# Optimization experiments

Hardware: AMD Instinct MI355X
Metric: run time of the kernel (lower is better)

Reference implementation:

```python
import jax, jax.numpy as jnp
import numpy as np

BS, C_IN, S1 = 64, 256, 32
D_OUT, J = 32, 10          # out_dim, num_out_caps (as_final_output -> spatial_size_2)
I = S1 * S1                # num_in_caps = 1024
ROUTE_NUM = 3


def setup_inputs() -> dict:
    key = jax.random.key(0)
    k1, k2, k3 = jax.random.split(key, 3)
    x = jax.random.normal(k1, (BS, C_IN, S1, S1), dtype=jnp.float32)
    W = jax.random.normal(k2, (D_OUT * J, C_IN), dtype=jnp.float32) * 0.02  # 1x1 conv weight
    W_b = jax.random.normal(k3, (D_OUT * J,), dtype=jnp.float32) * 0.02     # conv bias
    return {"x": x, "W": W, "W_b": W_b}


def squash(vec):
    # vec: [bs, j, d]; coeff = ||v||^2 / (1+||v||^2) / ||v||
    norm = jnp.linalg.norm(vec, axis=2, keepdims=True)
    norm_sq = norm * norm
    return vec * (norm_sq / (1.0 + norm_sq) / norm)


def reference(x, W, W_b):
    bs = x.shape[0]
    # 1x1 conv == per-pixel matmul: [bs, J*D, h, w]
    pred = jnp.einsum('bchw,oc->bohw', x, W) + W_b[None, :, None, None]
    # torch: resize(bs, J, D, I) on contiguous tensor, then permute(0,3,1,2)
    pred = pred.reshape(bs, J, D_OUT, I).transpose(0, 3, 1, 2)  # [bs, I, J, D]
    b = jnp.zeros((bs, J, I), dtype=x.dtype)  # b_init='zero'
    v = None
    for _ in range(ROUTE_NUM):
        c = jax.nn.softmax(b, axis=1)                    # softmax over output caps j
        s = jnp.einsum('bji,bijd->bjd', c, pred)          # per-capsule weighted sum
        v = squash(s)                                     # [bs, J, D]
        delta_b = jnp.einsum('bjd,bijd->bji', v, pred)    # agreement
        b = b + jax.lax.stop_gradient(delta_b)            # torch .detach()
    return v  # as_final_output=True -> [bs, J, D]
```

## Files before the change

kernel.cpp:

```cpp
#include <hip/hip_runtime.h>
#include <hip/hip_bf16.h>

typedef __attribute__((ext_vector_type(8))) unsigned short u16x8;
typedef __attribute__((ext_vector_type(4))) unsigned short u16x4;
typedef __attribute__((ext_vector_type(8))) short short8;
typedef __attribute__((ext_vector_type(4))) float floatx4;

#define BS 64
#define CIN 256
#define II 1024
#define OO 320
#define JJ 10
#define DD 32

__device__ __forceinline__ float b2f(unsigned short u) {
    union { unsigned int i; float f; } x; x.i = ((unsigned int)u) << 16; return x.f;
}
__device__ __forceinline__ unsigned short f2b(float f) {
    union { float f; unsigned int i; } x; x.f = f;
    unsigned int r = x.i + 0x7fffu + ((x.i >> 16) & 1u);
    return (unsigned short)(r >> 16);
}

__device__ __forceinline__ float butterfly32(const float* p, int l) {
    float q16[16];
#pragma unroll
    for (int d = 0; d < 16; ++d) {
        float keep = (l & 1) ? p[2 * d + 1] : p[2 * d];
        float send = (l & 1) ? p[2 * d] : p[2 * d + 1];
        q16[d] = keep + __shfl_xor(send, 1);
    }
    float q8[8];
#pragma unroll
    for (int d = 0; d < 8; ++d) {
        float keep = (l & 2) ? q16[2 * d + 1] : q16[2 * d];
        float send = (l & 2) ? q16[2 * d] : q16[2 * d + 1];
        q8[d] = keep + __shfl_xor(send, 2);
    }
    float q4[4];
#pragma unroll
    for (int d = 0; d < 4; ++d) {
        float keep = (l & 4) ? q8[2 * d + 1] : q8[2 * d];
        float send = (l & 4) ? q8[2 * d] : q8[2 * d + 1];
        q4[d] = keep + __shfl_xor(send, 4);
    }
    float q2[2];
#pragma unroll
    for (int d = 0; d < 2; ++d) {
        float keep = (l & 8) ? q4[2 * d + 1] : q4[2 * d];
        float send = (l & 8) ? q4[2 * d] : q4[2 * d + 1];
        q2[d] = keep + __shfl_xor(send, 8);
    }
    float keep = (l & 16) ? q2[1] : q2[0];
    float send = (l & 16) ? q2[0] : q2[1];
    float q1 = keep + __shfl_xor(send, 16);
    q1 += __shfl_xor(q1, 32);
    return q1;
}

__global__ __launch_bounds__(256) void k_prepW(const float* __restrict__ W,
                                               unsigned short* __restrict__ Wl) {
    int gid = blockIdx.x * 256 + threadIdx.x;
    int lm = gid & 15;
    int quad = (gid >> 4) & 3;
    int mtl = (gid >> 6) & 3;
    int ks = (gid >> 8) & 7;
    int oc = gid >> 11;
    const float* src = W + (size_t)(oc * 64 + mtl * 16 + lm) * CIN + ks * 32 + quad * 8;
    float4 v0 = *(const float4*)src;
    float4 v1 = *(const float4*)(src + 4);
    u16x8 u;
    u[0] = f2b(v0.x); u[1] = f2b(v0.y); u[2] = f2b(v0.z); u[3] = f2b(v0.w);
    u[4] = f2b(v1.x); u[5] = f2b(v1.y); u[6] = f2b(v1.z); u[7] = f2b(v1.w);
    *(u16x8*)(Wl + (size_t)gid * 8) = u;
}

__global__ __launch_bounds__(512) void k_gemm8(const float* __restrict__ x,
                                               const unsigned short* __restrict__ Wl,
                                               const float* __restrict__ Wb,
                                               unsigned short* __restrict__ pred,
                                               float* __restrict__ psumC) {
    __shared__ unsigned short buf[2][16896];
    __shared__ float Wb_lds[OO];

    const int ic = blockIdx.x, b = blockIdx.y;
    const int t = threadIdx.x, w = t >> 6, l = t & 63;
    const int lm = l & 15, quad = l >> 4;
    const int i0 = ic * 128;

    if (t < OO) Wb_lds[t] = Wb[t];

    {
        const u16x8* src = (const u16x8*)Wl;
        u16x8* dst = (u16x8*)buf[1];
        dst[t] = src[t];
        dst[t + 512] = src[t + 512];
        dst[t + 1024] = src[t + 1024];
        dst[t + 1536] = src[t + 1536];
    }

    short8 bfrag[8];
    float csum[2];
    const int crow = t >> 5, f4 = t & 31;
    const int cs_c = t >> 2, cs_seg = t & 3;
#pragma unroll
    for (int kc = 0; kc < 2; ++kc) {
        float4 fr[8];
#pragma unroll
        for (int p = 0; p < 8; ++p) {
            int c = kc * 128 + p * 16 + crow;
            fr[p] = *(const float4*)(x + ((size_t)b * CIN + c) * II + i0 + 4 * f4);
        }
#pragma unroll
        for (int p = 0; p < 8; ++p) {
            int cl = p * 16 + crow;
            u16x4 u;
            u[0] = f2b(fr[p].x); u[1] = f2b(fr[p].y); u[2] = f2b(fr[p].z); u[3] = f2b(fr[p].w);
            *(u16x4*)&buf[0][cl * 132 + 4 * f4] = u;
        }
        __syncthreads();
#pragma unroll
        for (int k2 = 0; k2 < 4; ++k2) {
            short8 f;
#pragma unroll
            for (int j = 0; j < 8; ++j)
                f[j] = (short)buf[0][(k2 * 32 + quad * 8 + j) * 132 + w * 16 + lm];
            bfrag[kc * 4 + k2] = f;
        }
        {
            float cs = 0.f;
#pragma unroll
            for (int q = 0; q < 8; ++q) {
                u16x4 u = *(const u16x4*)&buf[0][cs_c * 132 + cs_seg * 32 + q * 4];
                cs += b2f(u[0]) + b2f(u[1]) + b2f(u[2]) + b2f(u[3]);
            }
            cs += __shfl_xor(cs, 1);
            cs += __shfl_xor(cs, 2);
            csum[kc] = cs;
        }
        __syncthreads();
    }
    if (cs_seg == 0) {
        size_t cbase = ((size_t)ic * BS + b) * CIN;
        psumC[cbase + cs_c] = csum[0];
        psumC[cbase + 128 + cs_c] = csum[1];
    }

    const size_t predrow = ((size_t)b * II + i0 + w * 16 + lm) * OO;
#pragma unroll 1
    for (int oc = 0; oc < 5; ++oc) {
        if (oc < 4) {
            const u16x8* src = (const u16x8*)Wl + (size_t)(oc + 1) * 2048;
            u16x8* dst = (u16x8*)buf[oc & 1];
            dst[t] = src[t];
            dst[t + 512] = src[t + 512];
            dst[t + 1024] = src[t + 1024];
            dst[t + 1536] = src[t + 1536];
        }
        const unsigned short* ab = buf[(oc + 1) & 1];
        floatx4 acc[4] = {};
#pragma unroll
        for (int ks = 0; ks < 8; ++ks)
#pragma unroll
            for (int mtl = 0; mtl < 4; ++mtl) {
                short8 af = *(const short8*)(ab + (size_t)(((ks * 4 + mtl) * 4 + quad) * 16 + lm) * 8);
                acc[mtl] = __builtin_amdgcn_mfma_f32_16x16x32_bf16(af, bfrag[ks], acc[mtl], 0, 0, 0);
            }
#pragma unroll
        for (int mtl = 0; mtl < 4; ++mtl) {
            int ob = oc * 64 + mtl * 16 + quad * 4;
            u16x4 sv;
#pragma unroll
            for (int r = 0; r < 4; ++r) sv[r] = f2b(acc[mtl][r] + Wb_lds[ob + r]);
            *(u16x4*)(pred + predrow + ob) = sv;
        }
        __syncthreads();
    }
}

__global__ __launch_bounds__(320) void k_gemv(const float* __restrict__ psumC,
                                              const float* __restrict__ W,
                                              const float* __restrict__ Wb,
                                              float* __restrict__ s1) {
    __shared__ float y_lds[CIN];
    const int b = blockIdx.x, t = threadIdx.x;
    if (t < CIN) {
        float s = 0.f;
#pragma unroll
        for (int sl = 0; sl < 8; ++sl) s += psumC[((size_t)sl * BS + b) * CIN + t];
        y_lds[t] = s;
    }
    __syncthreads();
    const float* wr = W + (size_t)t * CIN;
    float acc = 0.f;
#pragma unroll 4
    for (int c = 0; c < CIN; c += 4) {
        float4 wv = *(const float4*)(wr + c);
        acc += wv.x * y_lds[c] + wv.y * y_lds[c + 1] + wv.z * y_lds[c + 2] + wv.w * y_lds[c + 3];
    }
    s1[(size_t)b * OO + t] = 0.1f * (acc + 1024.0f * Wb[t]);
}

__global__ __launch_bounds__(640) void k_route1(const float* __restrict__ s1,
                                                const unsigned short* __restrict__ pred,
                                                float* __restrict__ blogG,
                                                float* __restrict__ psum1) {
    __shared__ float s_lds[OO];
    __shared__ float v_lds[OO];
    __shared__ float cf[JJ];
    __shared__ float dbuf[JJ][128];

    const int ic = blockIdx.x, b = blockIdx.y;
    const int t = threadIdx.x, w = t >> 6, l = t & 63;

    u16x8 va[4], vb[4];
    {
        const unsigned short* p0 = pred + ((size_t)b * II + ic * 128 + 2 * l) * OO + w * DD;
#pragma unroll
        for (int q = 0; q < 4; ++q) {
            va[q] = *(const u16x8*)(p0 + q * 8);
            vb[q] = *(const u16x8*)(p0 + OO + q * 8);
        }
    }

    if (t < OO) s_lds[t] = s1[(size_t)b * OO + t];
    __syncthreads();
    if (t < JJ) {
        float n2 = 0.f;
#pragma unroll
        for (int d = 0; d < DD; ++d) { float v = s_lds[t * DD + d]; n2 += v * v; }
        cf[t] = sqrtf(n2) / (1.0f + n2);
    }
    __syncthreads();
    if (t < OO) v_lds[t] = s_lds[t] * cf[t >> 5];
    __syncthreads();

    float d0 = 0.f, d1 = 0.f;
#pragma unroll
    for (int q = 0; q < 4; ++q)
#pragma unroll
        for (int e = 0; e < 8; ++e) {
            float vv = v_lds[w * DD + q * 8 + e];
            d0 += vv * b2f(va[q][e]);
            d1 += vv * b2f(vb[q][e]);
        }
    *(float2*)(blogG + ((size_t)b * JJ + w) * II + ic * 128 + 2 * l) = make_float2(d0, d1);
    dbuf[w][2 * l] = d0; dbuf[w][2 * l + 1] = d1;
    __syncthreads();

    if (t < 128) {
        float lg[JJ];
#pragma unroll
        for (int j = 0; j < JJ; ++j) lg[j] = dbuf[j][t];
        float m = lg[0];
#pragma unroll
        for (int j = 1; j < JJ; ++j) m = fmaxf(m, lg[j]);
        float Z = 0.f, c[JJ];
#pragma unroll
        for (int j = 0; j < JJ; ++j) { c[j] = __expf(lg[j] - m); Z += c[j]; }
        float inv = 1.0f / Z;
#pragma unroll
        for (int j = 0; j < JJ; ++j) dbuf[j][t] = c[j] * inv;
    }
    __syncthreads();

    float c0 = dbuf[w][2 * l], c1 = dbuf[w][2 * l + 1];
    float p[DD];
#pragma unroll
    for (int q = 0; q < 4; ++q)
#pragma unroll
        for (int e = 0; e < 8; ++e)
            p[q * 8 + e] = c0 * b2f(va[q][e]) + c1 * b2f(vb[q][e]);
    float s = butterfly32(p, l);
    if (l < 32) psum1[((size_t)ic * BS + b) * OO + w * DD + l] = s;
}

__global__ __launch_bounds__(640) void k_route2(const float* __restrict__ psum1,
                                                const unsigned short* __restrict__ pred,
                                                const float* __restrict__ blogG,
                                                float* __restrict__ psum2) {
    __shared__ float s_lds[OO];
    __shared__ float v_lds[OO];
    __shared__ float cf[JJ];
    __shared__ float dbuf[JJ][128];

    const int ic = blockIdx.x, b = blockIdx.y;
    const int t = threadIdx.x, w = t >> 6, l = t & 63;

    u16x8 va[4], vb[4];
    {
        const unsigned short* p0 = pred + ((size_t)b * II + ic * 128 + 2 * l) * OO + w * DD;
#pragma unroll
        for (int q = 0; q < 4; ++q) {
            va[q] = *(const u16x8*)(p0 + q * 8);
            vb[q] = *(const u16x8*)(p0 + OO + q * 8);
        }
    }

    if (t < OO) {
        float s = 0.f;
#pragma unroll
        for (int sl = 0; sl < 8; ++sl) s += psum1[((size_t)sl * BS + b) * OO + t];
        s_lds[t] = s;
    }
    __syncthreads();
    if (t < JJ) {
        float n2 = 0.f;
#pragma unroll
        for (int d = 0; d < DD; ++d) { float v = s_lds[t * DD + d]; n2 += v * v; }
        cf[t] = sqrtf(n2) / (1.0f + n2);
    }
    __syncthreads();
    if (t < OO) v_lds[t] = s_lds[t] * cf[t >> 5];
    __syncthreads();

    float d0 = 0.f, d1 = 0.f;
#pragma unroll
    for (int q = 0; q < 4; ++q)
#pragma unroll
        for (int e = 0; e < 8; ++e) {
            float vv = v_lds[w * DD + q * 8 + e];
            d0 += vv * b2f(va[q][e]);
            d1 += vv * b2f(vb[q][e]);
        }
    float2 bl = *(const float2*)(blogG + ((size_t)b * JJ + w) * II + ic * 128 + 2 * l);
    dbuf[w][2 * l] = bl.x + d0; dbuf[w][2 * l + 1] = bl.y + d1;
    __syncthreads();

    if (t < 128) {
        float lg[JJ];
#pragma unroll
        for (int j = 0; j < JJ; ++j) lg[j] = dbuf[j][t];
        float m = lg[0];
#pragma unroll
        for (int j = 1; j < JJ; ++j) m = fmaxf(m, lg[j]);
        float Z = 0.f, c[JJ];
#pragma unroll
        for (int j = 0; j < JJ; ++j) { c[j] = __expf(lg[j] - m); Z += c[j]; }
        float inv = 1.0f / Z;
#pragma unroll
        for (int j = 0; j < JJ; ++j) dbuf[j][t] = c[j] * inv;
    }
    __syncthreads();

    float c0 = dbuf[w][2 * l], c1 = dbuf[w][2 * l + 1];
    float p[DD];
#pragma unroll
    for (int q = 0; q < 4; ++q)
#pragma unroll
        for (int e = 0; e < 8; ++e)
            p[q * 8 + e] = c0 * b2f(va[q][e]) + c1 * b2f(vb[q][e]);
    float s = butterfly32(p, l);
    if (l < 32) psum2[((size_t)ic * BS + b) * OO + w * DD + l] = s;
}

__global__ __launch_bounds__(320) void k_final2(const float* __restrict__ psum2,
                                                float* __restrict__ out) {
    __shared__ float s_lds[OO];
    __shared__ float cf[JJ];
    int b = blockIdx.x, t = threadIdx.x;
    float s = 0.f;
#pragma unroll
    for (int sl = 0; sl < 8; ++sl) s += psum2[((size_t)sl * BS + b) * OO + t];
    s_lds[t] = s;
    __syncthreads();
    if (t < JJ) {
        float n2 = 0.f;
#pragma unroll
        for (int d = 0; d < DD; ++d) { float v = s_lds[t * DD + d]; n2 += v * v; }
        cf[t] = sqrtf(n2) / (1.0f + n2);
    }
    __syncthreads();
    out[b * OO + t] = s_lds[t] * cf[t >> 5];
}

extern "C" void kernel_launch(void* const* d_in, const int* in_sizes, int n_in,
                              void* d_out, int out_size, void* d_ws, size_t ws_size,
                              hipStream_t stream) {
    const float* x  = (const float*)d_in[0];
    const float* W  = (const float*)d_in[1];
    const float* Wb = (const float*)d_in[2];

    char* ws = (char*)d_ws;
    unsigned short* pred = (unsigned short*)ws;
    unsigned short* Wl   = (unsigned short*)(ws + 41943040);
    float* psumC = (float*)(ws + 42106880);
    float* s1    = (float*)(ws + 42631168);
    float* psum1 = (float*)(ws + 42713088);
    float* psum2 = (float*)(ws + 43368448);
    float* blogG = (float*)(ws + 44023808);

    k_prepW<<<40, 256, 0, stream>>>(W, Wl);
    k_gemm8<<<dim3(8, BS), 512, 0, stream>>>(x, Wl, Wb, pred, psumC);
    k_gemv<<<BS, 320, 0, stream>>>(psumC, W, Wb, s1);
    k_route1<<<dim3(8, BS), 640, 0, stream>>>(s1, pred, blogG, psum1);
    k_route2<<<dim3(8, BS), 640, 0, stream>>>(psum1, pred, blogG, psum2);
    k_final2<<<BS, 320, 0, stream>>>(psum2, (float*)d_out);
}
```

Baseline: 152.2 us.

## Fuse GEMM and routing iterations into one cooperative persistent kernel

Adds a cooperative megakernel that computes the 1x1-conv GEMM, keeps each block's bf16 predictions packed in registers, and runs both routing passes plus the final squash with grid-wide syncs between stages. This avoids writing and re-reading the large pred tensor in global memory, and it replaces several kernel launches with one. The first-iteration sum now comes from per-block partials of pred rather than a separate GEMV. The costs are three grid syncs, higher register pressure from holding 40 packed values per thread, and a reliance on all 512 blocks being co-resident. If the cooperative launch fails, the old kernel sequence runs instead.

```diff
diff --git a/kernel.cpp b/kernel.cpp
--- a/kernel.cpp
+++ b/kernel.cpp
@@ -1,5 +1,8 @@
 #include <hip/hip_runtime.h>
 #include <hip/hip_bf16.h>
+#include <hip/hip_cooperative_groups.h>
+
+namespace cg = cooperative_groups;
 
 typedef __attribute__((ext_vector_type(8))) unsigned short u16x8;
 typedef __attribute__((ext_vector_type(4))) unsigned short u16x4;
@@ -56,6 +59,33 @@
     float q1 = keep + __shfl_xor(send, 16);
     q1 += __shfl_xor(q1, 32);
     return q1;
+}
+
+__device__ __forceinline__ float butterfly16(const float* p, int l) {
+    float q8[8];
+#pragma unroll
+    for (int d = 0; d < 8; ++d) {
+        float keep = (l & 1) ? p[2 * d + 1] : p[2 * d];
+        float send = (l & 1) ? p[2 * d] : p[2 * d + 1];
+        q8[d] = keep + __shfl_xor(send, 1);
+    }
+    float q4[4];
+#pragma unroll
+    for (int d = 0; d < 4; ++d) {
+        float keep = (l & 2) ? q8[2 * d + 1] : q8[2 * d];
+        float send = (l & 2) ? q8[2 * d] : q8[2 * d + 1];
+        q4[d] = keep + __shfl_xor(send, 2);
+    }
+    float q2[2];
+#pragma unroll
+    for (int d = 0; d < 2; ++d) {
+        float keep = (l & 4) ? q4[2 * d + 1] : q4[2 * d];
+        float send = (l & 4) ? q4[2 * d] : q4[2 * d + 1];
+        q2[d] = keep + __shfl_xor(send, 4);
+    }
+    float keep = (l & 8) ? q2[1] : q2[0];
+    float send = (l & 8) ? q2[0] : q2[1];
+    return keep + __shfl_xor(send, 8);
 }
 
 __global__ __launch_bounds__(256) void k_prepW(const float* __restrict__ W,
@@ -75,6 +105,202 @@
     *(u16x8*)(Wl + (size_t)gid * 8) = u;
 }
 
+
+__device__ __forceinline__ void route_pass(
+        const float* __restrict__ srcpart, float scale, bool first,
+        const unsigned* pk, float* b_reg, float* __restrict__ dstpart,
+        float* sacc, float* v_lds, float* cf,
+        int ic, int b, int t, int l, int lm, int quad) {
+    if (t < OO) {
+        float s = 0.f;
+#pragma unroll
+        for (int sl = 0; sl < 8; ++sl) s += srcpart[((size_t)sl * BS + b) * OO + t];
+        sacc[t] = scale * s;
+    }
+    __syncthreads();
+    if (t < JJ) {
+        float n2 = 0.f;
+#pragma unroll
+        for (int d = 0; d < DD; ++d) { float v = sacc[t * DD + d]; n2 += v * v; }
+        cf[t] = sqrtf(n2) / (1.0f + n2);
+    }
+    __syncthreads();
+    if (t < OO) { v_lds[t] = sacc[t] * cf[t >> 5]; sacc[t] = 0.f; }
+    __syncthreads();
+
+    float dj[JJ];
+#pragma unroll
+    for (int j = 0; j < JJ; ++j) dj[j] = 0.f;
+#pragma unroll
+    for (int m = 0; m < 20; ++m) {
+        float4 vv = *(const float4*)&v_lds[m * 16 + quad * 4];
+        unsigned a0 = pk[2 * m], a1 = pk[2 * m + 1];
+        dj[m >> 1] += b2f((unsigned short)(a0 & 0xffffu)) * vv.x
+                    + b2f((unsigned short)(a0 >> 16)) * vv.y
+                    + b2f((unsigned short)(a1 & 0xffffu)) * vv.z
+                    + b2f((unsigned short)(a1 >> 16)) * vv.w;
+    }
+#pragma unroll
+    for (int j = 0; j < JJ; ++j) {
+        float d = dj[j];
+        d += __shfl_xor(d, 16);
+        d += __shfl_xor(d, 32);
+        b_reg[j] = first ? d : (b_reg[j] + d);
+    }
+    float mx = b_reg[0];
+#pragma unroll
+    for (int j = 1; j < JJ; ++j) mx = fmaxf(mx, b_reg[j]);
+    float cj[JJ], Z = 0.f;
+#pragma unroll
+    for (int j = 0; j < JJ; ++j) { cj[j] = __expf(b_reg[j] - mx); Z += cj[j]; }
+    float inv = 1.0f / Z;
+#pragma unroll
+    for (int g = 0; g < 5; ++g) {
+        float v16[16];
+#pragma unroll
+        for (int mm = 0; mm < 4; ++mm) {
+            int m = 4 * g + mm;
+            unsigned a0 = pk[2 * m], a1 = pk[2 * m + 1];
+            float c = cj[m >> 1] * inv;
+            v16[4 * mm + 0] = c * b2f((unsigned short)(a0 & 0xffffu));
+            v16[4 * mm + 1] = c * b2f((unsigned short)(a0 >> 16));
+            v16[4 * mm + 2] = c * b2f((unsigned short)(a1 & 0xffffu));
+            v16[4 * mm + 3] = c * b2f((unsigned short)(a1 >> 16));
+        }
+        float q = butterfly16(v16, l);
+        atomicAdd(&sacc[g * 64 + (lm >> 2) * 16 + quad * 4 + (lm & 3)], q);
+    }
+    __syncthreads();
+    if (t < OO) dstpart[((size_t)ic * BS + b) * OO + t] = sacc[t];
+}
+
+__global__ __launch_bounds__(512, 4) void k_mega(
+        const float* __restrict__ x, const unsigned short* __restrict__ Wl,
+        const float* __restrict__ Wb, float* __restrict__ s1part,
+        float* __restrict__ psum1, float* __restrict__ psum2,
+        float* __restrict__ out) {
+    __shared__ unsigned short buf[2][16896];
+    __shared__ float Wb_lds[OO];
+    __shared__ float sacc[OO];
+    __shared__ __align__(16) float v_lds[OO];
+    __shared__ float cf[16];
+
+    cg::grid_group gg = cg::this_grid();
+
+    const int ic = blockIdx.x, b = blockIdx.y;
+    const int t = threadIdx.x, w = t >> 6, l = t & 63;
+    const int lm = l & 15, quad = l >> 4;
+    const int i0 = ic * 128;
+
+    if (t < OO) { Wb_lds[t] = Wb[t]; sacc[t] = 0.f; }
+
+    {
+        const u16x8* src = (const u16x8*)Wl;
+        u16x8* dst = (u16x8*)buf[1];
+        dst[t] = src[t];
+        dst[t + 512] = src[t + 512];
+        dst[t + 1024] = src[t + 1024];
+        dst[t + 1536] = src[t + 1536];
+    }
+
+    short8 bfrag[8];
+    const int crow = t >> 5, f4 = t & 31;
+#pragma unroll
+    for (int kc = 0; kc < 2; ++kc) {
+        float4 fr[8];
+#pragma unroll
+        for (int p = 0; p < 8; ++p) {
+            int c = kc * 128 + p * 16 + crow;
+            fr[p] = *(const float4*)(x + ((size_t)b * CIN + c) * II + i0 + 4 * f4);
+        }
+#pragma unroll
+        for (int p = 0; p < 8; ++p) {
+            int cl = p * 16 + crow;
+            u16x4 u;
+            u[0] = f2b(fr[p].x); u[1] = f2b(fr[p].y); u[2] = f2b(fr[p].z); u[3] = f2b(fr[p].w);
+            *(u16x4*)&buf[0][cl * 132 + 4 * f4] = u;
+        }
+        __syncthreads();
+#pragma unroll
+        for (int k2 = 0; k2 < 4; ++k2) {
+            short8 f;
+#pragma unroll
+            for (int j = 0; j < 8; ++j)
+                f[j] = (short)buf[0][(k2 * 32 + quad * 8 + j) * 132 + w * 16 + lm];
+            bfrag[kc * 4 + k2] = f;
+        }
+        __syncthreads();
+    }
+
+    unsigned pk[40];
+#pragma unroll
+    for (int oc = 0; oc < 5; ++oc) {
+        if (oc < 4) {
+            const u16x8* src = (const u16x8*)Wl + (size_t)(oc + 1) * 2048;
+            u16x8* dst = (u16x8*)buf[oc & 1];
+            dst[t] = src[t];
+            dst[t + 512] = src[t + 512];
+            dst[t + 1024] = src[t + 1024];
+            dst[t + 1536] = src[t + 1536];
+        }
+        const unsigned short* ab = buf[(oc + 1) & 1];
+        floatx4 acc[4] = {};
+#pragma unroll
+        for (int ks = 0; ks < 8; ++ks)
+#pragma unroll
+            for (int mtl = 0; mtl < 4; ++mtl) {
+                short8 af = *(const short8*)(ab + (size_t)(((ks * 4 + mtl) * 4 + quad) * 16 + lm) * 8);
+                acc[mtl] = __builtin_amdgcn_mfma_f32_16x16x32_bf16(af, bfrag[ks], acc[mtl], 0, 0, 0);
+            }
+        float av[16];
+#pragma unroll
+        for (int mtl = 0; mtl < 4; ++mtl) {
+            int ob = oc * 64 + mtl * 16 + quad * 4;
+#pragma unroll
+            for (int r = 0; r < 4; ++r) av[mtl * 4 + r] = acc[mtl][r] + Wb_lds[ob + r];
+            pk[oc * 8 + mtl * 2 + 0] =
+                (unsigned)f2b(av[mtl * 4 + 0]) | ((unsigned)f2b(av[mtl * 4 + 1]) << 16);
+            pk[oc * 8 + mtl * 2 + 1] =
+                (unsigned)f2b(av[mtl * 4 + 2]) | ((unsigned)f2b(av[mtl * 4 + 3]) << 16);
+        }
+        float q = butterfly16(av, l);
+        atomicAdd(&sacc[oc * 64 + (lm >> 2) * 16 + quad * 4 + (lm & 3)], q);
+        __syncthreads();
+    }
+
+    if (t < OO) s1part[((size_t)ic * BS + b) * OO + t] = sacc[t];
+    __threadfence();
+    gg.sync();
+
+    float b_reg[JJ];
+    route_pass(s1part, 0.1f, true, pk, b_reg, psum1, sacc, v_lds, cf, ic, b, t, l, lm, quad);
+    __threadfence();
+    gg.sync();
+
+    route_pass(psum1, 1.0f, false, pk, b_reg, psum2, sacc, v_lds, cf, ic, b, t, l, lm, quad);
+    __threadfence();
+    gg.sync();
+
+    if (ic == 0) {
+        if (t < OO) {
+            float s = 0.f;
+#pragma unroll
+            for (int sl = 0; sl < 8; ++sl) s += psum2[((size_t)sl * BS + b) * OO + t];
+            sacc[t] = s;
+        }
+        __syncthreads();
+        if (t < JJ) {
+            float n2 = 0.f;
+#pragma unroll
+            for (int d = 0; d < DD; ++d) { float v = sacc[t * DD + d]; n2 += v * v; }
+            cf[t] = sqrtf(n2) / (1.0f + n2);
+        }
+        __syncthreads();
+        if (t < OO) out[b * OO + t] = sacc[t] * cf[t >> 5];
+    }
+}
+
+
 __global__ __launch_bounds__(512) void k_gemm8(const float* __restrict__ x,
                                                const unsigned short* __restrict__ Wl,
                                                const float* __restrict__ Wb,
@@ -389,8 +615,24 @@
     float* psum1 = (float*)(ws + 42713088);
     float* psum2 = (float*)(ws + 43368448);
     float* blogG = (float*)(ws + 44023808);
+    float* s1part = (float*)(ws + 46645248);
 
     k_prepW<<<40, 256, 0, stream>>>(W, Wl);
+
+    {
+        const float* a0 = x;
+        const unsigned short* a1 = Wl;
+        const float* a2 = Wb;
+        float* a3 = s1part;
+        float* a4 = psum1;
+        float* a5 = psum2;
+        float* a6 = (float*)d_out;
+        void* kargs[] = {&a0, &a1, &a2, &a3, &a4, &a5, &a6};
+        hipError_t e = hipLaunchCooperativeKernel(k_mega, dim3(8, BS), dim3(512, 1, 1),
+                                                  kargs, 0, stream);
+        if (e == hipSuccess) return;
+    }
+
     k_gemm8<<<dim3(8, BS), 512, 0, stream>>>(x, Wl, Wb, pred, psumC);
     k_gemv<<<BS, 320, 0, stream>>>(psumC, W, Wb, s1);
     k_route1<<<dim3(8, BS), 640, 0, stream>>>(s1, pred, blogG, psum1);
```

Result: slower. 471.7 us (+209.9%).

## Reorder bf16 pred layout so GEMM stores and routing loads are coalesced

Applied to the files above, without the earlier changes.

The GEMM epilogue now writes pred in a blocked layout: per (batch, 128-capsule chunk), groups of 4 output channels by 128 capsules, each capsule's 4 channels contiguous. The two routing kernels read this layout with 8 strided 16-byte loads whose lanes are adjacent in memory, replacing the row-major [i][320] reads that strode 640 bytes between lanes. The aim is fully coalesced global traffic for the pred tensor, which is written once and read twice. The index math has to stay consistent between producer and consumers.

```diff
diff --git a/kernel.cpp b/kernel.cpp
--- a/kernel.cpp
+++ b/kernel.cpp
@@ -75,6 +75,7 @@
     *(u16x8*)(Wl + (size_t)gid * 8) = u;
 }
 
+
 __global__ __launch_bounds__(512) void k_gemm8(const float* __restrict__ x,
                                                const unsigned short* __restrict__ Wl,
                                                const float* __restrict__ Wb,
@@ -146,7 +147,7 @@
         psumC[cbase + 128 + cs_c] = csum[1];
     }
 
-    const size_t predrow = ((size_t)b * II + i0 + w * 16 + lm) * OO;
+    const size_t predbase = ((size_t)(b * 8 + ic)) * 40960 + (size_t)(w * 16 + lm) * 4;
 #pragma unroll 1
     for (int oc = 0; oc < 5; ++oc) {
         if (oc < 4) {
@@ -169,10 +170,11 @@
 #pragma unroll
         for (int mtl = 0; mtl < 4; ++mtl) {
             int ob = oc * 64 + mtl * 16 + quad * 4;
+            int mprime = oc * 16 + mtl * 4 + quad;
             u16x4 sv;
 #pragma unroll
             for (int r = 0; r < 4; ++r) sv[r] = f2b(acc[mtl][r] + Wb_lds[ob + r]);
-            *(u16x4*)(pred + predrow + ob) = sv;
+            *(u16x4*)(pred + predbase + (size_t)mprime * 512) = sv;
         }
         __syncthreads();
     }
@@ -213,14 +215,13 @@
     const int ic = blockIdx.x, b = blockIdx.y;
     const int t = threadIdx.x, w = t >> 6, l = t & 63;
 
-    u16x8 va[4], vb[4];
+    u16x8 Ld[8];
     {
-        const unsigned short* p0 = pred + ((size_t)b * II + ic * 128 + 2 * l) * OO + w * DD;
-#pragma unroll
-        for (int q = 0; q < 4; ++q) {
-            va[q] = *(const u16x8*)(p0 + q * 8);
-            vb[q] = *(const u16x8*)(p0 + OO + q * 8);
-        }
+        const unsigned short* p0 = pred + ((size_t)(b * 8 + ic)) * 40960
+                                 + (size_t)(w * 8) * 512 + 8 * l;
+#pragma unroll
+        for (int dq = 0; dq < 8; ++dq)
+            Ld[dq] = *(const u16x8*)(p0 + (size_t)dq * 512);
     }
 
     if (t < OO) s_lds[t] = s1[(size_t)b * OO + t];
@@ -237,12 +238,12 @@
 
     float d0 = 0.f, d1 = 0.f;
 #pragma unroll
-    for (int q = 0; q < 4; ++q)
-#pragma unroll
-        for (int e = 0; e < 8; ++e) {
-            float vv = v_lds[w * DD + q * 8 + e];
-            d0 += vv * b2f(va[q][e]);
-            d1 += vv * b2f(vb[q][e]);
+    for (int dq = 0; dq < 8; ++dq)
+#pragma unroll
+        for (int e = 0; e < 4; ++e) {
+            float vv = v_lds[w * DD + dq * 4 + e];
+            d0 += vv * b2f(Ld[dq][e]);
+            d1 += vv * b2f(Ld[dq][4 + e]);
         }
     *(float2*)(blogG + ((size_t)b * JJ + w) * II + ic * 128 + 2 * l) = make_float2(d0, d1);
     dbuf[w][2 * l] = d0; dbuf[w][2 * l + 1] = d1;
@@ -267,10 +268,10 @@
     float c0 = dbuf[w][2 * l], c1 = dbuf[w][2 * l + 1];
     float p[DD];
 #pragma unroll
-    for (int q = 0; q < 4; ++q)
-#pragma unroll
-        for (int e = 0; e < 8; ++e)
-            p[q * 8 + e] = c0 * b2f(va[q][e]) + c1 * b2f(vb[q][e]);
+    for (int dq = 0; dq < 8; ++dq)
+#pragma unroll
+        for (int e = 0; e < 4; ++e)
+            p[dq * 4 + e] = c0 * b2f(Ld[dq][e]) + c1 * b2f(Ld[dq][4 + e]);
     float s = butterfly32(p, l);
     if (l < 32) psum1[((size_t)ic * BS + b) * OO + w * DD + l] = s;
 }
@@ -287,14 +288,13 @@
     const int ic = blockIdx.x, b = blockIdx.y;
     const int t = threadIdx.x, w = t >> 6, l = t & 63;
 
-    u16x8 va[4], vb[4];
+    u16x8 Ld[8];
     {
-        const unsigned short* p0 = pred + ((size_t)b * II + ic * 128 + 2 * l) * OO + w * DD;
-#pragma unroll
-        for (int q = 0; q < 4; ++q) {
-            va[q] = *(const u16x8*)(p0 + q * 8);
-            vb[q] = *(const u16x8*)(p0 + OO + q * 8);
-        }
+        const unsigned short* p0 = pred + ((size_t)(b * 8 + ic)) * 40960
+                                 + (size_t)(w * 8) * 512 + 8 * l;
+#pragma unroll
+        for (int dq = 0; dq < 8; ++dq)
+            Ld[dq] = *(const u16x8*)(p0 + (size_t)dq * 512);
     }
 
     if (t < OO) {
@@ -316,12 +316,12 @@
 
     float d0 = 0.f, d1 = 0.f;
 #pragma unroll
-    for (int q = 0; q < 4; ++q)
-#pragma unroll
-        for (int e = 0; e < 8; ++e) {
-            float vv = v_lds[w * DD + q * 8 + e];
-            d0 += vv * b2f(va[q][e]);
-            d1 += vv * b2f(vb[q][e]);
+    for (int dq = 0; dq < 8; ++dq)
+#pragma unroll
+        for (int e = 0; e < 4; ++e) {
+            float vv = v_lds[w * DD + dq * 4 + e];
+            d0 += vv * b2f(Ld[dq][e]);
+            d1 += vv * b2f(Ld[dq][4 + e]);
         }
     float2 bl = *(const float2*)(blogG + ((size_t)b * JJ + w) * II + ic * 128 + 2 * l);
     dbuf[w][2 * l] = bl.x + d0; dbuf[w][2 * l + 1] = bl.y + d1;
@@ -346,10 +346,10 @@
     float c0 = dbuf[w][2 * l], c1 = dbuf[w][2 * l + 1];
     float p[DD];
 #pragma unroll
-    for (int q = 0; q < 4; ++q)
-#pragma unroll
-        for (int e = 0; e < 8; ++e)
-            p[q * 8 + e] = c0 * b2f(va[q][e]) + c1 * b2f(vb[q][e]);
+    for (int dq = 0; dq < 8; ++dq)
+#pragma unroll
+        for (int e = 0; e < 4; ++e)
+            p[dq * 4 + e] = c0 * b2f(Ld[dq][e]) + c1 * b2f(Ld[dq][4 + e]);
     float s = butterfly32(p, l);
     if (l < 32) psum2[((size_t)ic * BS + b) * OO + w * DD + l] = s;
 }
```

Measured after the change: 146.8 us (median of 2 runs). 3.6% less time.
